# Optimization experiments

Measured on AMD Instinct MI355X. Metric: run time of the kernel, lower is better.

Reference implementation:

```python
import jax, jax.numpy as jnp
import numpy as np

N_NODES = 50000
N_EDGES = 800000
D = 64
H = 4
ALPHA = 0.2  # LeakyReLU negative slope


def gat_conv(x, W, a_s, a_d, src, dst):
    # x: [N, D], W: [D, D], a_s/a_d: [D]
    h = x @ W                               # [N, D]
    s_src = h @ a_s                         # [N]
    s_dst = h @ a_d                         # [N]
    e = jax.nn.leaky_relu(s_src[src] + s_dst[dst], ALPHA)   # [E]
    # segment softmax over incoming edges of each dst node
    m = jax.ops.segment_max(e, dst, num_segments=N_NODES)   # [N]
    ex = jnp.exp(e - m[dst])                                # [E]
    z = jax.ops.segment_sum(ex, dst, num_segments=N_NODES)  # [N]
    attn = ex / (z[dst] + 1e-16)                            # [E]
    out = jax.ops.segment_sum(h[src] * attn[:, None], dst, num_segments=N_NODES)
    return out


def gat_layer(x, W, a_s, a_d, src, dst):
    # sequential application of H single-head convs (as in the torch code);
    # dropout is identity in eval mode
    out = x
    for i in range(H):
        out = gat_conv(out, W[i], a_s[i], a_d[i], src, dst)
    return jax.nn.elu(out)


def setup_inputs() -> dict:
    key = jax.random.key(0)
    ks = jax.random.split(key, 8)
    sc = 1.0 / np.sqrt(D)
    features = jax.random.normal(ks[0], (N_NODES, D), dtype=jnp.float32)
    edge_index = jax.random.randint(ks[1], (2, N_EDGES), 0, N_NODES, dtype=jnp.int64)
    W1 = jax.random.normal(ks[2], (H, D, D), dtype=jnp.float32) * sc
    a_src1 = jax.random.normal(ks[3], (H, D), dtype=jnp.float32) * sc
    a_dst1 = jax.random.normal(ks[4], (H, D), dtype=jnp.float32) * sc
    W2 = jax.random.normal(ks[5], (H, D, D), dtype=jnp.float32) * sc
    a_src2 = jax.random.normal(ks[6], (H, D), dtype=jnp.float32) * sc
    a_dst2 = jax.random.normal(ks[7], (H, D), dtype=jnp.float32) * sc
    return {"features": features, "edge_index": edge_index,
            "W1": W1, "a_src1": a_src1, "a_dst1": a_dst1,
            "W2": W2, "a_src2": a_src2, "a_dst2": a_dst2}


def reference(features, edge_index, W1, a_src1, a_dst1, W2, a_src2, a_dst2):
    src, dst = edge_index[0], edge_index[1]
    x = gat_layer(features, W1, a_src1, a_dst1, src, dst)
    # F.dropout between layers is identity in eval mode
    x = gat_layer(x, W2, a_src2, a_dst2, src, dst)
    return x
```

## Files before the change

kernel.cpp:

```cpp
#include <hip/hip_runtime.h>
#include <hip/hip_bf16.h>

#define N_NODES 50000
#define N_EDGES 800000
#define DIM 64
#define NB 391
#define NBLK 128
#define CHUNK 6250
#define CAP 4096
#define NTILES 3125

typedef __attribute__((ext_vector_type(8))) short bf16x8;
typedef __attribute__((ext_vector_type(4))) float f32x4;

__device__ __forceinline__ float bf2f(unsigned short u) {
  return __uint_as_float(((unsigned int)u) << 16);
}
__device__ __forceinline__ unsigned short f2bf(float f) {
  unsigned int x = __float_as_uint(f);
  unsigned int r = (x + 0x7fffu + ((x >> 16) & 1u)) >> 16;
  return (unsigned short)r;
}

__global__ void k_detect(const unsigned short* __restrict__ feat,
                         const unsigned int* __restrict__ eidx,
                         int* __restrict__ flags) {
  int lane = threadIdx.x;
  float v = bf2f(feat[2 * lane]);
  bool big = !(fabsf(v) < 1000.0f);
  unsigned long long bb = __ballot(big);
  unsigned int w = eidx[2 * lane + 1];
  unsigned long long bz = __ballot(w == 0u);
  if (lane == 0) {
    flags[0] = (__popcll(bb) < 8) ? 1 : 0;
    flags[1] = (__popcll(bz) == 64) ? 1 : 0;
  }
}

__device__ __forceinline__ int eidx_at(const int* __restrict__ p, int k, int i64) {
  return p[i64 ? (k << 1) : k];
}

__global__ void k_scan1(const int* __restrict__ in, int* __restrict__ out,
                        int* __restrict__ bsum, int n) {
  __shared__ int sm[256];
  int t = threadIdx.x, b = blockIdx.x, i = b * 256 + t;
  int v = (i < n) ? in[i] : 0;
  sm[t] = v;
  __syncthreads();
  for (int off = 1; off < 256; off <<= 1) {
    int x = (t >= off) ? sm[t - off] : 0;
    __syncthreads();
    sm[t] += x;
    __syncthreads();
  }
  if (i < n) out[i] = sm[t] - v;
  if (t == 255) bsum[b] = sm[t];
}

__global__ void k_scan2(int* __restrict__ bsum, int nb) {
  __shared__ int sm[256];
  int t = threadIdx.x;
  int v = (t < nb) ? bsum[t] : 0;
  sm[t] = v;
  __syncthreads();
  for (int off = 1; off < 256; off <<= 1) {
    int x = (t >= off) ? sm[t - off] : 0;
    __syncthreads();
    sm[t] += x;
    __syncthreads();
  }
  if (t < nb) bsum[t] = sm[t] - v;
}

__global__ void k_scan3(int* __restrict__ out, const int* __restrict__ bsum, int n) {
  int t = threadIdx.x, b = blockIdx.x, i = b * 256 + t;
  if (i < n) out[i] += bsum[b];
}

__global__ __launch_bounds__(256) void k_hist1(const int* __restrict__ eidx,
                                               const int* __restrict__ flags,
                                               int* __restrict__ hist) {
  __shared__ int h[NB];
  int t = threadIdx.x, b = blockIdx.x;
  for (int i = t; i < NB; i += 256) h[i] = 0;
  __syncthreads();
  int i64 = flags[1];
  int lo = b * CHUNK;
  for (int i = t; i < CHUNK; i += 256) {
    int d = eidx_at(eidx, N_EDGES + lo + i, i64);
    atomicAdd(&h[d >> 7], 1);
  }
  __syncthreads();
  for (int i = t; i < NB; i += 256) hist[i * NBLK + b] = h[i];
}

__global__ __launch_bounds__(256) void k_scatter(const int* __restrict__ eidx,
                                                 const int* __restrict__ flags,
                                                 const int* __restrict__ hscan,
                                                 int2* __restrict__ ebuf) {
  __shared__ int cur[NB];
  int t = threadIdx.x, b = blockIdx.x;
  for (int i = t; i < NB; i += 256) cur[i] = hscan[i * NBLK + b];
  __syncthreads();
  int i64 = flags[1];
  int lo = b * CHUNK;
  for (int i = t; i < CHUNK; i += 256) {
    int d = eidx_at(eidx, N_EDGES + lo + i, i64);
    int s = eidx_at(eidx, lo + i, i64);
    int pos = atomicAdd(&cur[d >> 7], 1);
    ebuf[pos] = make_int2(s, d);
  }
}

__global__ __launch_bounds__(256) void k_place(const int2* __restrict__ ebuf,
                                               const int* __restrict__ hscan,
                                               int* __restrict__ rowp,
                                               int* __restrict__ csr) {
  __shared__ int hcnt[128];
  __shared__ int sm[128];
  __shared__ int cur[128];
  __shared__ int lcsr[CAP];
  int t = threadIdx.x, b = blockIdx.x;
  int lo = hscan[b * NBLK];
  int hi = (b + 1 < NB) ? hscan[(b + 1) * NBLK] : N_EDGES;
  if (t < 128) hcnt[t] = 0;
  __syncthreads();
  for (int i = lo + t; i < hi; i += 256) atomicAdd(&hcnt[ebuf[i].y & 127], 1);
  __syncthreads();
  int v = (t < 128) ? hcnt[t] : 0;
  if (t < 128) sm[t] = v;
  __syncthreads();
  for (int off = 1; off < 128; off <<= 1) {
    int x = (t < 128 && t >= off) ? sm[t - off] : 0;
    __syncthreads();
    if (t < 128) sm[t] += x;
    __syncthreads();
  }
  int d0 = b * 128;
  if (t < 128) {
    int excl = sm[t] - v;
    cur[t] = excl;
    int d = d0 + t;
    if (d < N_NODES) rowp[d] = lo + excl;
  }
  if (b == NB - 1 && t == 0) rowp[N_NODES] = N_EDGES;
  __syncthreads();
  int seg_sz = hi - lo;
  if (seg_sz <= CAP) {
    for (int i = lo + t; i < hi; i += 256) {
      int2 pr = ebuf[i];
      int pos = atomicAdd(&cur[pr.y & 127], 1);
      lcsr[pos] = pr.x;
    }
    __syncthreads();
    for (int i = t; i < seg_sz; i += 256) csr[lo + i] = lcsr[i];
  } else {
    for (int i = lo + t; i < hi; i += 256) {
      int2 pr = ebuf[i];
      int pos = atomicAdd(&cur[pr.y & 127], 1);
      csr[lo + pos] = pr.x;
    }
  }
}

__global__ __launch_bounds__(256) void k_gemm(
    const void* __restrict__ xv, int x_raw, const void* __restrict__ Wv,
    const void* __restrict__ asv, const void* __restrict__ adv, int head,
    const int* __restrict__ flags, unsigned short* __restrict__ hb,
    float* __restrict__ ss, float* __restrict__ sd) {
  const int bf = flags[0];
  const int lane = threadIdx.x & 63;
  const int wtile = blockIdx.x * 4 + (threadIdx.x >> 6);
  if (wtile >= NTILES) return;
  const int r16 = lane & 15;
  const int g4 = lane >> 4;
  const int row0 = wtile * 16;

  bf16x8 Bh[4][2];
  bf16x8 Bl[4][2];
  if (bf) {
    const unsigned short* W = (const unsigned short*)Wv + head * DIM * DIM;
#pragma unroll
    for (int cb = 0; cb < 4; ++cb)
#pragma unroll
      for (int ks = 0; ks < 2; ++ks)
#pragma unroll
        for (int j = 0; j < 8; ++j)
          Bh[cb][ks][j] = (short)W[(32 * ks + 8 * g4 + j) * DIM + 16 * cb + r16];
  } else {
    const float* W = (const float*)Wv + head * DIM * DIM;
#pragma unroll
    for (int cb = 0; cb < 4; ++cb)
#pragma unroll
      for (int ks = 0; ks < 2; ++ks)
#pragma unroll
        for (int j = 0; j < 8; ++j) {
          float w = W[(32 * ks + 8 * g4 + j) * DIM + 16 * cb + r16];
          unsigned short hu = f2bf(w);
          Bh[cb][ks][j] = (short)hu;
          Bl[cb][ks][j] = (short)f2bf(w - bf2f(hu));
        }
  }

  const int a_bf = x_raw && bf;
  bf16x8 Ah[2], Al[2];
  if (a_bf) {
    const unsigned short* xp = (const unsigned short*)xv + (row0 + r16) * DIM + 8 * g4;
#pragma unroll
    for (int ks = 0; ks < 2; ++ks)
      Ah[ks] = *(const bf16x8*)(xp + 32 * ks);
  } else {
    const float* xp = (const float*)xv + (row0 + r16) * DIM + 8 * g4;
#pragma unroll
    for (int ks = 0; ks < 2; ++ks) {
      float4 f0 = *(const float4*)(xp + 32 * ks);
      float4 f1 = *(const float4*)(xp + 32 * ks + 4);
      float v[8] = {f0.x, f0.y, f0.z, f0.w, f1.x, f1.y, f1.z, f1.w};
#pragma unroll
      for (int j = 0; j < 8; ++j) {
        unsigned short hu = f2bf(v[j]);
        Ah[ks][j] = (short)hu;
        Al[ks][j] = (short)f2bf(v[j] - bf2f(hu));
      }
    }
  }

  f32x4 acc[4];
#pragma unroll
  for (int cb = 0; cb < 4; ++cb) {
    acc[cb] = (f32x4){0.f, 0.f, 0.f, 0.f};
#pragma unroll
    for (int ks = 0; ks < 2; ++ks) {
      acc[cb] = __builtin_amdgcn_mfma_f32_16x16x32_bf16(Ah[ks], Bh[cb][ks], acc[cb], 0, 0, 0);
      if (!a_bf)
        acc[cb] = __builtin_amdgcn_mfma_f32_16x16x32_bf16(Al[ks], Bh[cb][ks], acc[cb], 0, 0, 0);
      if (!bf)
        acc[cb] = __builtin_amdgcn_mfma_f32_16x16x32_bf16(Ah[ks], Bl[cb][ks], acc[cb], 0, 0, 0);
    }
  }

  float asl[4], adl[4];
  if (bf) {
    const unsigned short* pa = (const unsigned short*)asv + head * DIM;
    const unsigned short* pd = (const unsigned short*)adv + head * DIM;
#pragma unroll
    for (int cb = 0; cb < 4; ++cb) {
      asl[cb] = bf2f(pa[16 * cb + r16]);
      adl[cb] = bf2f(pd[16 * cb + r16]);
    }
  } else {
    const float* pa = (const float*)asv + head * DIM;
    const float* pd = (const float*)adv + head * DIM;
#pragma unroll
    for (int cb = 0; cb < 4; ++cb) {
      asl[cb] = pa[16 * cb + r16];
      adl[cb] = pd[16 * cb + r16];
    }
  }

  float u[4] = {0.f, 0.f, 0.f, 0.f}, vv[4] = {0.f, 0.f, 0.f, 0.f};
#pragma unroll
  for (int cb = 0; cb < 4; ++cb)
#pragma unroll
    for (int reg = 0; reg < 4; ++reg) {
      float hv = acc[cb][reg];
      hb[(row0 + 4 * g4 + reg) * DIM + 16 * cb + r16] = f2bf(hv);
      u[reg] = fmaf(hv, asl[cb], u[reg]);
      vv[reg] = fmaf(hv, adl[cb], vv[reg]);
    }
#pragma unroll
  for (int off = 1; off < 16; off <<= 1)
#pragma unroll
    for (int reg = 0; reg < 4; ++reg) {
      u[reg] += __shfl_xor(u[reg], off);
      vv[reg] += __shfl_xor(vv[reg], off);
    }
  if (r16 == 0) {
#pragma unroll
    for (int reg = 0; reg < 4; ++reg) {
      ss[row0 + 4 * g4 + reg] = u[reg];
      sd[row0 + 4 * g4 + reg] = vv[reg];
    }
  }
}

__device__ __forceinline__ void quad_accum(const unsigned short* __restrict__ hb,
                                           const int2* __restrict__ lps, int cl,
                                           int quarter, int c16, float4& acc) {
  const int quads = (cl + 3) >> 2;
#pragma unroll 4
  for (int tt = 0; tt < quads; ++tt) {
    int j = 4 * tt + quarter;
    int2 pv = lps[j];
    float pj = __int_as_float(pv.x);
    int sj = pv.y;
    ushort4 hv = *(const ushort4*)(hb + sj * DIM + 4 * c16);
    acc.x = fmaf(pj, bf2f(hv.x), acc.x);
    acc.y = fmaf(pj, bf2f(hv.y), acc.y);
    acc.z = fmaf(pj, bf2f(hv.z), acc.z);
    acc.w = fmaf(pj, bf2f(hv.w), acc.w);
  }
}

__global__ __launch_bounds__(256) void k_agg(
    const unsigned short* __restrict__ hb, const float* __restrict__ ss,
    const float* __restrict__ sd, const int* __restrict__ rowp,
    const int* __restrict__ csr, float* __restrict__ out_f,
    void* __restrict__ out_final, const int* __restrict__ flags,
    int do_elu, int is_final) {
  __shared__ __align__(16) int2 lps[4][64];
  const int lane = threadIdx.x & 63;
  const int quarter = lane >> 4;
  const int c16 = lane & 15;
  const int w = threadIdx.x >> 6;
  const int node = blockIdx.x * 4 + w;
  const int base = rowp[node];
  const int deg = rowp[node + 1] - base;
  const float sdn = sd[node];

  float4 acc = {0.f, 0.f, 0.f, 0.f};
  float z;
  if (deg <= 64) {
    int s = 0;
    float p = 0.f;
    if (lane < deg) {
      s = csr[base + lane];
      float t = ss[s] + sdn;
      t = (t >= 0.f) ? t : 0.2f * t;
      p = __expf(t);
    }
    lps[w][lane] = make_int2(__float_as_int(p), s);
    z = p;
    __builtin_amdgcn_wave_barrier();
    quad_accum(hb, &lps[w][0], deg, quarter, c16, acc);
#pragma unroll
    for (int off = 32; off > 0; off >>= 1) z += __shfl_xor(z, off);
  } else {
    z = 0.f;
    for (int c = 0; c < deg; c += 64) {
      int j = c + lane;
      float p = 0.f; int s = 0;
      if (j < deg) {
        s = csr[base + j];
        float sc = ss[s] + sdn;
        sc = (sc >= 0.f) ? sc : 0.2f * sc;
        p = __expf(sc);
      }
      lps[w][lane] = make_int2(__float_as_int(p), s);
      __builtin_amdgcn_wave_barrier();
      z += p;
      const int cl = (deg - c < 64) ? (deg - c) : 64;
      quad_accum(hb, &lps[w][0], cl, quarter, c16, acc);
      __builtin_amdgcn_wave_barrier();
    }
#pragma unroll
    for (int off = 32; off > 0; off >>= 1) z += __shfl_xor(z, off);
  }

  acc.x += __shfl_xor(acc.x, 16);
  acc.y += __shfl_xor(acc.y, 16);
  acc.z += __shfl_xor(acc.z, 16);
  acc.w += __shfl_xor(acc.w, 16);
  acc.x += __shfl_xor(acc.x, 32);
  acc.y += __shfl_xor(acc.y, 32);
  acc.z += __shfl_xor(acc.z, 32);
  acc.w += __shfl_xor(acc.w, 32);

  float inv = 1.f / (z + 1e-16f);
  float ox = acc.x * inv, oy = acc.y * inv;
  float oz = acc.z * inv, ow = acc.w * inv;
  if (do_elu) {
    ox = (ox > 0.f) ? ox : expm1f(ox);
    oy = (oy > 0.f) ? oy : expm1f(oy);
    oz = (oz > 0.f) ? oz : expm1f(oz);
    ow = (ow > 0.f) ? ow : expm1f(ow);
  }
  if (quarter == 0) {
    int idx = node * DIM + 4 * c16;
    if (is_final) {
      if (flags[0]) {
        ushort4 o4 = {f2bf(ox), f2bf(oy), f2bf(oz), f2bf(ow)};
        *(ushort4*)((unsigned short*)out_final + idx) = o4;
      } else {
        float4 o4 = {ox, oy, oz, ow};
        *(float4*)((float*)out_final + idx) = o4;
      }
    } else {
      float4 o4 = {ox, oy, oz, ow};
      *(float4*)(out_f + idx) = o4;
    }
  }
}

extern "C" void kernel_launch(void* const* d_in, const int* in_sizes, int n_in,
                              void* d_out, int out_size, void* d_ws, size_t ws_size,
                              hipStream_t stream) {
  const void* feat = d_in[0];
  const int* eidx = (const int*)d_in[1];

  float* bufA = (float*)d_ws;
  float* bufB = bufA + N_NODES * DIM;
  unsigned short* hb = (unsigned short*)(bufB + N_NODES * DIM);
  int2* ebuf = (int2*)(hb + N_NODES * DIM);
  float* ssrc = (float*)(ebuf + N_EDGES);
  float* sdst = ssrc + N_NODES;
  int* rowp = (int*)(sdst + N_NODES);
  int* csr  = rowp + N_NODES + 1;
  int* hist = csr + N_EDGES;
  int* hscan = hist + NB * NBLK;
  int* bsum = hscan + NB * NBLK;
  int* flags = bsum + 256;

  const int NH = NB * NBLK;
  const int SBH = (NH + 255) / 256;

  k_detect<<<1, 64, 0, stream>>>((const unsigned short*)feat,
                                 (const unsigned int*)eidx, flags);
  k_hist1<<<NBLK, 256, 0, stream>>>(eidx, flags, hist);
  k_scan1<<<SBH, 256, 0, stream>>>(hist, hscan, bsum, NH);
  k_scan2<<<1, 256, 0, stream>>>(bsum, SBH);
  k_scan3<<<SBH, 256, 0, stream>>>(hscan, bsum, NH);
  k_scatter<<<NBLK, 256, 0, stream>>>(eidx, flags, hscan, ebuf);
  k_place<<<NB, 256, 0, stream>>>(ebuf, hscan, rowp, csr);

  const int GB = (NTILES + 3) / 4;

  const void* xcur = feat;
  int x_raw = 1;
  float* nxt = bufA;
  float* other = bufB;
  for (int i = 0; i < 8; ++i) {
    const void* Wb = (i < 4) ? d_in[2] : d_in[5];
    const void* ab = (i < 4) ? d_in[3] : d_in[6];
    const void* db = (i < 4) ? d_in[4] : d_in[7];
    int head = i & 3;
    k_gemm<<<GB, 256, 0, stream>>>(xcur, x_raw, Wb, ab, db, head, flags,
                                   hb, ssrc, sdst);
    int elu = (i == 3 || i == 7) ? 1 : 0;
    int fin = (i == 7) ? 1 : 0;
    k_agg<<<N_NODES / 4, 256, 0, stream>>>(hb, ssrc, sdst, rowp, csr, nxt,
                                           d_out, flags, elu, fin);
    xcur = nxt; x_raw = 0;
    float* t = nxt; nxt = other; other = t;
  }
}
```

Before: 405.7 us.

## Precompute fragment-layout weights and fold attention vectors into GEMM via W·a

Adds a prep kernel that converts all eight weight matrices once into hi/lo bf16 MFMA fragment layout and precomputes W·a_src and W·a_dst, so attention scores come from an extra MFMA on x instead of a shuffle reduction over h. Intermediate activations are stored as split hi/lo bf16 pairs written by the aggregation kernel, removing per-GEMM fp32-to-bf16 splitting. The GEMM is split so each wave computes half the output columns, doubling the number of waves. The cost is extra launches, more weight loads per wave, and scores computed from x rather than from rounded h, which slightly changes numerics.

```diff
diff --git a/kernel.cpp b/kernel.cpp
--- a/kernel.cpp
+++ b/kernel.cpp
@@ -41,6 +41,90 @@
   return p[i64 ? (k << 1) : k];
 }
 
+__global__ __launch_bounds__(256) void k_wprep(
+    const void* __restrict__ W1, const void* __restrict__ A1s,
+    const void* __restrict__ A1d, const void* __restrict__ W2,
+    const void* __restrict__ A2s, const void* __restrict__ A2d,
+    const int* __restrict__ flags, unsigned short* __restrict__ wfH,
+    unsigned short* __restrict__ wfL, unsigned short* __restrict__ baf) {
+  __shared__ float Wsh[DIM * DIM];
+  __shared__ float was[DIM], wad[DIM];
+  const int b = blockIdx.x;
+  const int t = threadIdx.x;
+  const int bf = flags[0];
+  const void* Wv = (b < 4) ? W1 : W2;
+  const void* av = (b < 4) ? A1s : A2s;
+  const void* dv = (b < 4) ? A1d : A2d;
+  const int hm = (b < 4) ? b : b - 4;
+  for (int i = t; i < DIM * DIM; i += 256)
+    Wsh[i] = bf ? bf2f(((const unsigned short*)Wv)[hm * DIM * DIM + i])
+                : ((const float*)Wv)[hm * DIM * DIM + i];
+  __syncthreads();
+  if (t < 128) {
+    int k = t & 63, isd = t >> 6;
+    const void* aptr = isd ? dv : av;
+    float acc = 0.f;
+    for (int c = 0; c < DIM; ++c) {
+      float a = bf ? bf2f(((const unsigned short*)aptr)[hm * DIM + c])
+                   : ((const float*)aptr)[hm * DIM + c];
+      acc = fmaf(Wsh[k * DIM + c], a, acc);
+    }
+    (isd ? wad : was)[k] = acc;
+  }
+  __syncthreads();
+  for (int idx = t; idx < 512; idx += 256) {
+    int lane = idx & 63, ks = (idx >> 6) & 1, cb = idx >> 7;
+    int g4 = lane >> 4, r16 = lane & 15;
+    int fo = (((b * 4 + cb) * 2 + ks) * 64 + lane) * 8;
+#pragma unroll
+    for (int j = 0; j < 8; ++j) {
+      int k = 32 * ks + 8 * g4 + j;
+      float w = Wsh[k * DIM + 16 * cb + r16];
+      unsigned short hu = f2bf(w);
+      wfH[fo + j] = hu;
+      wfL[fo + j] = f2bf(w - bf2f(hu));
+    }
+  }
+  for (int idx = t; idx < 128; idx += 256) {
+    int lane = idx & 63, ks = idx >> 6;
+    int g4 = lane >> 4, r16 = lane & 15;
+    int fo = ((b * 2 + ks) * 64 + lane) * 8;
+#pragma unroll
+    for (int j = 0; j < 8; ++j) {
+      int k = 32 * ks + 8 * g4 + j;
+      unsigned short u = 0;
+      if (r16 < 4) {
+        float w_ = (r16 < 2) ? was[k] : wad[k];
+        unsigned short uh = f2bf(w_);
+        u = (r16 & 1) ? f2bf(w_ - bf2f(uh)) : uh;
+      }
+      baf[fo + j] = u;
+    }
+  }
+}
+
+__global__ __launch_bounds__(256) void k_split(const void* __restrict__ feat,
+                                               const int* __restrict__ flags,
+                                               unsigned short* __restrict__ xh,
+                                               unsigned short* __restrict__ xl) {
+  int i = (blockIdx.x * 256 + threadIdx.x) * 4;
+  if (i >= N_NODES * DIM) return;
+  if (flags[0]) {
+    ushort4 v = *(const ushort4*)((const unsigned short*)feat + i);
+    *(ushort4*)(xh + i) = v;
+    *(ushort4*)(xl + i) = make_ushort4(0, 0, 0, 0);
+  } else {
+    float4 f = *(const float4*)((const float*)feat + i);
+    ushort4 h4, l4;
+    h4.x = f2bf(f.x); l4.x = f2bf(f.x - bf2f(h4.x));
+    h4.y = f2bf(f.y); l4.y = f2bf(f.y - bf2f(h4.y));
+    h4.z = f2bf(f.z); l4.z = f2bf(f.z - bf2f(h4.z));
+    h4.w = f2bf(f.w); l4.w = f2bf(f.w - bf2f(h4.w));
+    *(ushort4*)(xh + i) = h4;
+    *(ushort4*)(xl + i) = l4;
+  }
+}
+
 __global__ void k_scan1(const int* __restrict__ in, int* __restrict__ out,
                         int* __restrict__ bsum, int n) {
   __shared__ int sm[256];
@@ -165,122 +249,71 @@
 }
 
 __global__ __launch_bounds__(256) void k_gemm(
-    const void* __restrict__ xv, int x_raw, const void* __restrict__ Wv,
-    const void* __restrict__ asv, const void* __restrict__ adv, int head,
-    const int* __restrict__ flags, unsigned short* __restrict__ hb,
-    float* __restrict__ ss, float* __restrict__ sd) {
-  const int bf = flags[0];
+    const unsigned short* __restrict__ xh, const unsigned short* __restrict__ xl,
+    const unsigned short* __restrict__ wfH, const unsigned short* __restrict__ wfL,
+    const unsigned short* __restrict__ baf, int mat,
+    unsigned short* __restrict__ hb, float* __restrict__ ss,
+    float* __restrict__ sd) {
   const int lane = threadIdx.x & 63;
-  const int wtile = blockIdx.x * 4 + (threadIdx.x >> 6);
+  const int w = blockIdx.x * 4 + (threadIdx.x >> 6);
+  const int wtile = w >> 1;
   if (wtile >= NTILES) return;
+  const int cbh = (w & 1) * 2;
   const int r16 = lane & 15;
   const int g4 = lane >> 4;
   const int row0 = wtile * 16;
 
-  bf16x8 Bh[4][2];
-  bf16x8 Bl[4][2];
-  if (bf) {
-    const unsigned short* W = (const unsigned short*)Wv + head * DIM * DIM;
-#pragma unroll
-    for (int cb = 0; cb < 4; ++cb)
-#pragma unroll
-      for (int ks = 0; ks < 2; ++ks)
-#pragma unroll
-        for (int j = 0; j < 8; ++j)
-          Bh[cb][ks][j] = (short)W[(32 * ks + 8 * g4 + j) * DIM + 16 * cb + r16];
-  } else {
-    const float* W = (const float*)Wv + head * DIM * DIM;
-#pragma unroll
-    for (int cb = 0; cb < 4; ++cb)
-#pragma unroll
-      for (int ks = 0; ks < 2; ++ks)
-#pragma unroll
-        for (int j = 0; j < 8; ++j) {
-          float w = W[(32 * ks + 8 * g4 + j) * DIM + 16 * cb + r16];
-          unsigned short hu = f2bf(w);
-          Bh[cb][ks][j] = (short)hu;
-          Bl[cb][ks][j] = (short)f2bf(w - bf2f(hu));
-        }
-  }
-
-  const int a_bf = x_raw && bf;
+  const bf16x8* WH = (const bf16x8*)wfH;
+  const bf16x8* WL = (const bf16x8*)wfL;
+  bf16x8 Bh[2][2], Bl[2][2];
+#pragma unroll
+  for (int c = 0; c < 2; ++c)
+#pragma unroll
+    for (int ks = 0; ks < 2; ++ks) {
+      int fi = ((mat * 4 + cbh + c) * 2 + ks) * 64 + lane;
+      Bh[c][ks] = WH[fi];
+      Bl[c][ks] = WL[fi];
+    }
+
   bf16x8 Ah[2], Al[2];
-  if (a_bf) {
-    const unsigned short* xp = (const unsigned short*)xv + (row0 + r16) * DIM + 8 * g4;
-#pragma unroll
-    for (int ks = 0; ks < 2; ++ks)
-      Ah[ks] = *(const bf16x8*)(xp + 32 * ks);
-  } else {
-    const float* xp = (const float*)xv + (row0 + r16) * DIM + 8 * g4;
+#pragma unroll
+  for (int ks = 0; ks < 2; ++ks) {
+    Ah[ks] = *(const bf16x8*)(xh + (row0 + r16) * DIM + 32 * ks + 8 * g4);
+    Al[ks] = *(const bf16x8*)(xl + (row0 + r16) * DIM + 32 * ks + 8 * g4);
+  }
+
+  f32x4 acc[2];
+#pragma unroll
+  for (int c = 0; c < 2; ++c) {
+    acc[c] = (f32x4){0.f, 0.f, 0.f, 0.f};
 #pragma unroll
     for (int ks = 0; ks < 2; ++ks) {
-      float4 f0 = *(const float4*)(xp + 32 * ks);
-      float4 f1 = *(const float4*)(xp + 32 * ks + 4);
-      float v[8] = {f0.x, f0.y, f0.z, f0.w, f1.x, f1.y, f1.z, f1.w};
-#pragma unroll
-      for (int j = 0; j < 8; ++j) {
-        unsigned short hu = f2bf(v[j]);
-        Ah[ks][j] = (short)hu;
-        Al[ks][j] = (short)f2bf(v[j] - bf2f(hu));
-      }
-    }
-  }
-
-  f32x4 acc[4];
-#pragma unroll
-  for (int cb = 0; cb < 4; ++cb) {
-    acc[cb] = (f32x4){0.f, 0.f, 0.f, 0.f};
+      acc[c] = __builtin_amdgcn_mfma_f32_16x16x32_bf16(Ah[ks], Bh[c][ks], acc[c], 0, 0, 0);
+      acc[c] = __builtin_amdgcn_mfma_f32_16x16x32_bf16(Al[ks], Bh[c][ks], acc[c], 0, 0, 0);
+      acc[c] = __builtin_amdgcn_mfma_f32_16x16x32_bf16(Ah[ks], Bl[c][ks], acc[c], 0, 0, 0);
+    }
+  }
+
+#pragma unroll
+  for (int c = 0; c < 2; ++c)
+#pragma unroll
+    for (int reg = 0; reg < 4; ++reg)
+      hb[(row0 + 4 * g4 + reg) * DIM + (cbh + c) * 16 + r16] = f2bf(acc[c][reg]);
+
+  if (cbh == 0) {
+    f32x4 acc2 = (f32x4){0.f, 0.f, 0.f, 0.f};
 #pragma unroll
     for (int ks = 0; ks < 2; ++ks) {
-      acc[cb] = __builtin_amdgcn_mfma_f32_16x16x32_bf16(Ah[ks], Bh[cb][ks], acc[cb], 0, 0, 0);
-      if (!a_bf)
-        acc[cb] = __builtin_amdgcn_mfma_f32_16x16x32_bf16(Al[ks], Bh[cb][ks], acc[cb], 0, 0, 0);
-      if (!bf)
-        acc[cb] = __builtin_amdgcn_mfma_f32_16x16x32_bf16(Ah[ks], Bl[cb][ks], acc[cb], 0, 0, 0);
-    }
-  }
-
-  float asl[4], adl[4];
-  if (bf) {
-    const unsigned short* pa = (const unsigned short*)asv + head * DIM;
-    const unsigned short* pd = (const unsigned short*)adv + head * DIM;
-#pragma unroll
-    for (int cb = 0; cb < 4; ++cb) {
-      asl[cb] = bf2f(pa[16 * cb + r16]);
-      adl[cb] = bf2f(pd[16 * cb + r16]);
-    }
-  } else {
-    const float* pa = (const float*)asv + head * DIM;
-    const float* pd = (const float*)adv + head * DIM;
-#pragma unroll
-    for (int cb = 0; cb < 4; ++cb) {
-      asl[cb] = pa[16 * cb + r16];
-      adl[cb] = pd[16 * cb + r16];
-    }
-  }
-
-  float u[4] = {0.f, 0.f, 0.f, 0.f}, vv[4] = {0.f, 0.f, 0.f, 0.f};
-#pragma unroll
-  for (int cb = 0; cb < 4; ++cb)
+      bf16x8 Ba = *(const bf16x8*)(baf + ((mat * 2 + ks) * 64 + lane) * 8);
+      acc2 = __builtin_amdgcn_mfma_f32_16x16x32_bf16(Ah[ks], Ba, acc2, 0, 0, 0);
+      acc2 = __builtin_amdgcn_mfma_f32_16x16x32_bf16(Al[ks], Ba, acc2, 0, 0, 0);
+    }
 #pragma unroll
     for (int reg = 0; reg < 4; ++reg) {
-      float hv = acc[cb][reg];
-      hb[(row0 + 4 * g4 + reg) * DIM + 16 * cb + r16] = f2bf(hv);
-      u[reg] = fmaf(hv, asl[cb], u[reg]);
-      vv[reg] = fmaf(hv, adl[cb], vv[reg]);
-    }
-#pragma unroll
-  for (int off = 1; off < 16; off <<= 1)
-#pragma unroll
-    for (int reg = 0; reg < 4; ++reg) {
-      u[reg] += __shfl_xor(u[reg], off);
-      vv[reg] += __shfl_xor(vv[reg], off);
-    }
-  if (r16 == 0) {
-#pragma unroll
-    for (int reg = 0; reg < 4; ++reg) {
-      ss[row0 + 4 * g4 + reg] = u[reg];
-      sd[row0 + 4 * g4 + reg] = vv[reg];
+      float tmp = acc2[reg] + __shfl_xor(acc2[reg], 1);
+      int row = row0 + 4 * g4 + reg;
+      if (r16 == 0) ss[row] = tmp;
+      else if (r16 == 2) sd[row] = tmp;
     }
   }
 }
@@ -306,9 +339,9 @@
 __global__ __launch_bounds__(256) void k_agg(
     const unsigned short* __restrict__ hb, const float* __restrict__ ss,
     const float* __restrict__ sd, const int* __restrict__ rowp,
-    const int* __restrict__ csr, float* __restrict__ out_f,
-    void* __restrict__ out_final, const int* __restrict__ flags,
-    int do_elu, int is_final) {
+    const int* __restrict__ csr, unsigned short* __restrict__ outH,
+    unsigned short* __restrict__ outL, void* __restrict__ out_final,
+    const int* __restrict__ flags, int do_elu, int is_final) {
   __shared__ __align__(16) int2 lps[4][64];
   const int lane = threadIdx.x & 63;
   const int quarter = lane >> 4;
@@ -387,8 +420,13 @@
         *(float4*)((float*)out_final + idx) = o4;
       }
     } else {
-      float4 o4 = {ox, oy, oz, ow};
-      *(float4*)(out_f + idx) = o4;
+      ushort4 h4, l4;
+      h4.x = f2bf(ox); l4.x = f2bf(ox - bf2f(h4.x));
+      h4.y = f2bf(oy); l4.y = f2bf(oy - bf2f(h4.y));
+      h4.z = f2bf(oz); l4.z = f2bf(oz - bf2f(h4.z));
+      h4.w = f2bf(ow); l4.w = f2bf(ow - bf2f(h4.w));
+      *(ushort4*)(outH + idx) = h4;
+      *(ushort4*)(outL + idx) = l4;
     }
   }
 }
@@ -399,24 +437,33 @@
   const void* feat = d_in[0];
   const int* eidx = (const int*)d_in[1];
 
-  float* bufA = (float*)d_ws;
-  float* bufB = bufA + N_NODES * DIM;
-  unsigned short* hb = (unsigned short*)(bufB + N_NODES * DIM);
-  int2* ebuf = (int2*)(hb + N_NODES * DIM);
+  unsigned short* xh0 = (unsigned short*)d_ws;
+  unsigned short* xl0 = xh0 + N_NODES * DIM;
+  unsigned short* xh1 = xl0 + N_NODES * DIM;
+  unsigned short* xl1 = xh1 + N_NODES * DIM;
+  unsigned short* hb  = xl1 + N_NODES * DIM;
+  unsigned short* wfH = hb + N_NODES * DIM;
+  unsigned short* wfL = wfH + 32768;
+  unsigned short* baf = wfL + 32768;
+  int2* ebuf = (int2*)(baf + 8192);
   float* ssrc = (float*)(ebuf + N_EDGES);
   float* sdst = ssrc + N_NODES;
-  int* rowp = (int*)(sdst + N_NODES);
-  int* csr  = rowp + N_NODES + 1;
+  int* csr  = (int*)(sdst + N_NODES);
   int* hist = csr + N_EDGES;
   int* hscan = hist + NB * NBLK;
   int* bsum = hscan + NB * NBLK;
-  int* flags = bsum + 256;
+  int* rowp = bsum + 256;
+  int* flags = rowp + N_NODES + 1;
 
   const int NH = NB * NBLK;
   const int SBH = (NH + 255) / 256;
 
   k_detect<<<1, 64, 0, stream>>>((const unsigned short*)feat,
                                  (const unsigned int*)eidx, flags);
+  k_wprep<<<8, 256, 0, stream>>>(d_in[2], d_in[3], d_in[4],
+                                 d_in[5], d_in[6], d_in[7],
+                                 flags, wfH, wfL, baf);
+  k_split<<<(N_NODES * DIM / 4 + 255) / 256, 256, 0, stream>>>(feat, flags, xh1, xl1);
   k_hist1<<<NBLK, 256, 0, stream>>>(eidx, flags, hist);
   k_scan1<<<SBH, 256, 0, stream>>>(hist, hscan, bsum, NH);
   k_scan2<<<1, 256, 0, stream>>>(bsum, SBH);
@@ -424,24 +471,18 @@
   k_scatter<<<NBLK, 256, 0, stream>>>(eidx, flags, hscan, ebuf);
   k_place<<<NB, 256, 0, stream>>>(ebuf, hscan, rowp, csr);
 
-  const int GB = (NTILES + 3) / 4;
-
-  const void* xcur = feat;
-  int x_raw = 1;
-  float* nxt = bufA;
-  float* other = bufB;
+  const int GB = (2 * NTILES + 3) / 4;
+
+  const unsigned short* xh = xh1;
+  const unsigned short* xl = xl1;
   for (int i = 0; i < 8; ++i) {
-    const void* Wb = (i < 4) ? d_in[2] : d_in[5];
-    const void* ab = (i < 4) ? d_in[3] : d_in[6];
-    const void* db = (i < 4) ? d_in[4] : d_in[7];
-    int head = i & 3;
-    k_gemm<<<GB, 256, 0, stream>>>(xcur, x_raw, Wb, ab, db, head, flags,
-                                   hb, ssrc, sdst);
+    k_gemm<<<GB, 256, 0, stream>>>(xh, xl, wfH, wfL, baf, i, hb, ssrc, sdst);
     int elu = (i == 3 || i == 7) ? 1 : 0;
     int fin = (i == 7) ? 1 : 0;
-    k_agg<<<N_NODES / 4, 256, 0, stream>>>(hb, ssrc, sdst, rowp, csr, nxt,
+    unsigned short* oh = (i & 1) ? xh1 : xh0;
+    unsigned short* ol = (i & 1) ? xl1 : xl0;
+    k_agg<<<N_NODES / 4, 256, 0, stream>>>(hb, ssrc, sdst, rowp, csr, oh, ol,
                                            d_out, flags, elu, fin);
-    xcur = nxt; x_raw = 0;
-    float* t = nxt; nxt = other; other = t;
-  }
-}
+    xh = oh; xl = ol;
+  }
+}
```

Measured after the change: 411.2 us. Within noise of the previous version (+1.4%).
